# Performance work log

Hardware: AMD Instinct MI355X
Metric: run time of the kernel (lower is better)

The kernel has to match this reference:

```python
import jax, jax.numpy as jnp
from jax import lax
import numpy as np

B, T, I, H, O = 2048, 512, 3, 128, 2


def _uniform(key, shape, scale):
    return jax.random.uniform(key, shape, jnp.float32, -scale, scale)


def setup_inputs() -> dict:
    key = jax.random.key(0)
    ks = jax.random.split(key, 12)
    s = 1.0 / np.sqrt(H)  # PyTorch LSTM init scale
    inp = {
        "x": jax.random.normal(ks[0], (B, T, I), jnp.float32),
        # layer 0: input size I
        "w_ih0": _uniform(ks[1], (4 * H, I), s),
        "w_hh0": _uniform(ks[2], (4 * H, H), s),
        "b_ih0": _uniform(ks[3], (4 * H,), s),
        "b_hh0": _uniform(ks[4], (4 * H,), s),
        # layer 1: input size H
        "w_ih1": _uniform(ks[5], (4 * H, H), s),
        "w_hh1": _uniform(ks[6], (4 * H, H), s),
        "b_ih1": _uniform(ks[7], (4 * H,), s),
        "b_hh1": _uniform(ks[8], (4 * H,), s),
        # final projection
        "fc_w": _uniform(ks[9], (O, H), 1.0 / np.sqrt(H)),
        "fc_b": _uniform(ks[10], (O,), 1.0 / np.sqrt(H)),
    }
    return inp


def _lstm_layer(x, w_ih, w_hh, b_ih, b_hh):
    # x: [B, T, D_in] -> hidden sequence [B, T, H]
    b, t, _ = x.shape
    h_dim = w_hh.shape[1]
    # precompute input projections for all timesteps (one big GEMM)
    x_proj = jnp.einsum("btd,gd->btg", x, w_ih) + b_ih + b_hh  # [B, T, 4H]
    x_proj = jnp.swapaxes(x_proj, 0, 1)  # [T, B, 4H]

    def step(carry, xt):
        h, c = carry
        gates = xt + h @ w_hh.T  # [B, 4H]
        i, f, g, o = jnp.split(gates, 4, axis=-1)  # PyTorch gate order i,f,g,o
        i = jax.nn.sigmoid(i)
        f = jax.nn.sigmoid(f)
        g = jnp.tanh(g)
        o = jax.nn.sigmoid(o)
        c = f * c + i * g
        h = o * jnp.tanh(c)
        return (h, c), h

    h0 = jnp.zeros((b, h_dim), x.dtype)
    c0 = jnp.zeros((b, h_dim), x.dtype)
    _, hs = lax.scan(step, (h0, c0), x_proj)  # hs: [T, B, H]
    return jnp.swapaxes(hs, 0, 1)  # [B, T, H]


def reference(x, w_ih0, w_hh0, b_ih0, b_hh0, w_ih1, w_hh1, b_ih1, b_hh1, fc_w, fc_b):
    h1 = _lstm_layer(x, w_ih0, w_hh0, b_ih0, b_hh0)   # [B, T, H]
    h2 = _lstm_layer(h1, w_ih1, w_hh1, b_ih1, b_hh1)  # [B, T, H]
    last = h2[:, -1, :]                                # [B, H]
    return last @ fc_w.T + fc_b                        # [B, O]
```

## Files before the change

### kernel.cpp

```cpp
#include <hip/hip_runtime.h>

#define B_   2048
#define T_   512
#define H_   128
#define G_   512
#define R_   8
#define NTHR 512

typedef _Float16 f16;
typedef _Float16 f16x8 __attribute__((ext_vector_type(8)));
typedef float    f32x4 __attribute__((ext_vector_type(4)));
typedef int      i32x2 __attribute__((ext_vector_type(2)));

#define OFF_W1    0
#define OFF_RING  131072
#define OFF_HB    139264
#define OFF_XT    143360
#define LDS_BYTES 145408

__device__ __forceinline__ float rcp_(float v) {
#if __has_builtin(__builtin_amdgcn_rcpf)
  return __builtin_amdgcn_rcpf(v);
#else
  return 1.0f / v;
#endif
}
__device__ __forceinline__ float sig_(float v)  { return rcp_(1.0f + __expf(-v)); }
__device__ __forceinline__ float tanh_(float v) { return 1.0f - 2.0f * rcp_(__expf(2.0f * v) + 1.0f); }

__device__ __forceinline__ f16x8 cvt8(const float* __restrict__ p) {
  float4 a = ((const float4*)p)[0];
  float4 b = ((const float4*)p)[1];
  f16x8 v;
  v[0]=(f16)a.x; v[1]=(f16)a.y; v[2]=(f16)a.z; v[3]=(f16)a.w;
  v[4]=(f16)b.x; v[5]=(f16)b.y; v[6]=(f16)b.z; v[7]=(f16)b.w;
  return v;
}
__device__ __forceinline__ f32x4 mfma16(f16x8 a, f16x8 b, f32x4 c) {
  return __builtin_amdgcn_mfma_f32_16x16x32_f16(a, b, c, 0, 0, 0);
}

__device__ __forceinline__ void pls2_(float a, float b, float& x, float& y) {
#if __has_builtin(__builtin_amdgcn_permlane32_swap)
  i32x2 r = __builtin_amdgcn_permlane32_swap(__float_as_int(a), __float_as_int(b),
                                             false, false);
  x = __int_as_float(r.x); y = __int_as_float(r.y);
#else
  asm volatile("v_permlane32_swap_b32 %0, %1" : "+v"(a), "+v"(b));
  x = a; y = b;
#endif
}

__global__ __launch_bounds__(NTHR, 2)
void lstm_v9(const float* __restrict__ x,
             const float* __restrict__ w_ih0, const float* __restrict__ w_hh0,
             const float* __restrict__ b_ih0, const float* __restrict__ b_hh0,
             const float* __restrict__ w_ih1, const float* __restrict__ w_hh1,
             const float* __restrict__ b_ih1, const float* __restrict__ b_hh1,
             const float* __restrict__ fc_w,  const float* __restrict__ fc_b,
             float* __restrict__ out)
{
  extern __shared__ char lds[];
  char*  w1L   = lds + OFF_W1;
  char*  ringB = lds + OFF_RING;
  char*  hBB   = lds + OFF_HB;
  char*  xT    = lds + OFF_XT;

  const int tid  = (int)threadIdx.x;
  const int lane = tid & 63;
  const int wv   = tid >> 6;
  const int n    = lane & 15;
  const int hi   = lane >> 4;
  const int u0   = wv * 16;
  const int blk  = (int)blockIdx.x;
  const int rsw  = (n & 7) << 4;

  for (int idx = tid; idx < G_*16; idx += NTHR) {
    const int g = idx >> 4, s7 = idx & 15;
    f16x8 v = cvt8(w_ih1 + g*H_ + s7*8);
    *(f16x8*)(w1L + g*256 + ((s7*16) ^ ((g&7)<<4))) = v;
  }
  for (int i = tid; i < 3584; i += NTHR) ((unsigned*)ringB)[i] = 0u;
  __syncthreads();

  float xr0 = 0.f, xr1 = 0.f, xr2 = 0.f;
  if (wv == 7) {
    const int tok = lane >> 3, r = lane & 7;
    const size_t base = (size_t)(blk*R_ + r) * T_;
    const float a0 = x[(base + tok)*3+0];
    const float a1 = x[(base + tok)*3+1];
    const float a2 = x[(base + tok)*3+2];
    f16* w = (f16*)(xT + tok*128 + r*16);
    w[0] = (f16)a0; w[1] = (f16)a1; w[2] = (f16)a2;
    xr0 = x[(base + 8 + tok)*3+0];
    xr1 = x[(base + 8 + tok)*3+1];
    xr2 = x[(base + 8 + tok)*3+2];
  }

  f16x8 whh0f[4][4], whh1f[4][4];
  #pragma unroll
  for (int q = 0; q < 4; ++q)
    #pragma unroll
    for (int kc = 0; kc < 4; ++kc) {
      const int off = (q*H_ + u0 + n)*H_ + kc*32 + hi*8;
      whh0f[q][kc] = cvt8(w_hh0 + off);
      whh1f[q][kc] = cvt8(w_hh1 + off);
    }
  f16x8 w0p[4];
  float b0[4], bP[4];
  #pragma unroll
  for (int q = 0; q < 4; ++q) {
    const int g = q*H_ + u0 + n;
    b0[q] = b_ih0[g] + b_hh0[g];
    bP[q] = b_ih1[g] + b_hh1[g];
    f16x8 z;
    #pragma unroll
    for (int e = 0; e < 8; ++e) z[e] = (f16)0.f;
    if (hi == 0) {
      z[0] = (f16)w_ih0[g*3+0];
      z[1] = (f16)w_ih0[g*3+1];
      z[2] = (f16)w_ih0[g*3+2];
    }
    w0p[q] = z;
  }

  int offA[4];
  #pragma unroll
  for (int kc = 0; kc < 4; ++kc)
    offA[kc] = (n&7)*256 + ((kc*64 + hi*16) ^ rsw);
  int offB[4];
  #pragma unroll
  for (int kc = 0; kc < 4; ++kc)
    offB[kc] = (kc*64 + hi*16) ^ rsw;

  float cA0 = 0.f, cA1 = 0.f, cB0 = 0.f, cB1 = 0.f;
  f32x4 xpP[4];
  const int rowbase = (hi & 1)*4 + ((lane >= 32) ? 2 : 0);
  const int colb    = 2*(u0 + n);
  const int wOff0 = rowbase*256     + (colb ^ (rowbase<<4));
  const int wOff1 = (rowbase+1)*256 + (colb ^ ((rowbase+1)<<4));
  __syncthreads();

  auto xstage = [&](int s) {
    if (wv == 7 && (s & 7) == 3) {
      const int c = s >> 3;
      const int tok = lane >> 3, r = lane & 7;
      if (c <= 61) {
        const size_t base = (size_t)(blk*R_ + r) * T_ + (8*(c+2) + tok);
        const float a0 = x[base*3+0], a1 = x[base*3+1], a2 = x[base*3+2];
        f16* w = (f16*)(xT + ((c+1)&1)*1024 + tok*128 + r*16);
        w[0] = (f16)xr0; w[1] = (f16)xr1; w[2] = (f16)xr2;
        xr0 = a0; xr1 = a1; xr2 = a2;
      } else if (c == 62) {
        f16* w = (f16*)(xT + ((c+1)&1)*1024 + tok*128 + r*16);
        w[0] = (f16)xr0; w[1] = (f16)xr1; w[2] = (f16)xr2;
      }
    }
  };

  auto proj = [&](int s) {
    if ((s & 1) == 0 && s >= 2 && s <= T_) {
      const char* pa = ringB + ((n < 8) ? (((s-2)&3)*2048) : (((s-1)&3)*2048));
      #pragma unroll
      for (int q = 0; q < 4; ++q)
        { xpP[q][0]=bP[q]; xpP[q][1]=bP[q]; xpP[q][2]=bP[q]; xpP[q][3]=bP[q]; }
      #pragma unroll
      for (int kc = 0; kc < 4; ++kc) {
        const f16x8 a = *(const f16x8*)(pa + offA[kc]);
        #pragma unroll
        for (int q = 0; q < 4; ++q) {
          const f16x8 bf = *(const f16x8*)(w1L + (q*H_ + u0 + n)*256 + offB[kc]);
          xpP[q] = mfma16(a, bf, xpP[q]);
        }
      }
    }
  };

  auto l0 = [&](int s) {
    if (s < T_) {
      const f16x8 ax = *(const f16x8*)(xT + ((s>>3)&1)*1024 + (s&7)*128 + (n&7)*16);
      f32x4 acc[4];
      #pragma unroll
      for (int q = 0; q < 4; ++q) {
        f32x4 a; a[0]=b0[q]; a[1]=b0[q]; a[2]=b0[q]; a[3]=b0[q];
        acc[q] = mfma16(ax, w0p[q], a);
      }
      const char* pa = ringB + (((s-1)&3)*2048);
      #pragma unroll
      for (int kc = 0; kc < 4; ++kc) {
        const f16x8 af = *(const f16x8*)(pa + offA[kc]);
        #pragma unroll
        for (int q = 0; q < 4; ++q) acc[q] = mfma16(af, whh0f[q][kc], acc[q]);
      }
      char* wr = ringB + ((s&3)*2048);
      float gA[4], gB[4], d0, d1;
      #pragma unroll
      for (int q = 0; q < 4; ++q) {
        pls2_(acc[q][0], acc[q][2], gA[q], d0);
        pls2_(acc[q][1], acc[q][3], gB[q], d1);
      }
      {
        const float iv = sig_(gA[0]), fv = sig_(gA[1]), gv = tanh_(gA[2]), ov = sig_(gA[3]);
        cA0 = fv*cA0 + iv*gv;
        *(f16*)(wr + wOff0) = (f16)(ov * tanh_(cA0));
      }
      {
        const float iv = sig_(gB[0]), fv = sig_(gB[1]), gv = tanh_(gB[2]), ov = sig_(gB[3]);
        cA1 = fv*cA1 + iv*gv;
        *(f16*)(wr + wOff1) = (f16)(ov * tanh_(cA1));
      }
    }
  };

  auto l1 = [&](int s) {
    if (s >= 2) {
      const bool odd = (s & 1);
      const char* pb = hBB + (s&1)*2048;
      f32x4 acc[4];
      #pragma unroll
      for (int q = 0; q < 4; ++q) acc[q] = xpP[q];
      #pragma unroll
      for (int kc = 0; kc < 4; ++kc) {
        const f16x8 af = *(const f16x8*)(pb + offA[kc]);
        #pragma unroll
        for (int q = 0; q < 4; ++q) acc[q] = mfma16(af, whh1f[q][kc], acc[q]);
      }
      char* wr = hBB + (((s+1)&1)*2048);
      float gA[4], gB[4];
      #pragma unroll
      for (int q = 0; q < 4; ++q) {
        float ex, ey, fx, fy;
        pls2_(acc[q][0], acc[q][2], ex, ey);
        pls2_(acc[q][1], acc[q][3], fx, fy);
        gA[q] = odd ? ey : ex;
        gB[q] = odd ? fy : fx;
      }
      {
        const float iv = sig_(gA[0]), fv = sig_(gA[1]), gv = tanh_(gA[2]), ov = sig_(gA[3]);
        cB0 = fv*cB0 + iv*gv;
        *(f16*)(wr + wOff0) = (f16)(ov * tanh_(cB0));
      }
      {
        const float iv = sig_(gB[0]), fv = sig_(gB[1]), gv = tanh_(gB[2]), ov = sig_(gB[3]);
        cB1 = fv*cB1 + iv*gv;
        *(f16*)(wr + wOff1) = (f16)(ov * tanh_(cB1));
      }
    }
  };

  for (int s = 0; s < T_ + 2; ++s) {
    if (wv & 1) {
      xstage(s);
      l0(s);
      proj(s);
      l1(s);
    } else {
      proj(s);
      l1(s);
      l0(s);
    }
    __syncthreads();
  }

  if (tid < R_*2) {
    const int r = tid >> 1, o = tid & 1;
    float acc = fc_b[o];
    #pragma unroll 4
    for (int d = 0; d < H_; ++d) {
      const f16 hv = *(const f16*)(hBB + r*256 + ((2*d) ^ ((r&7)<<4)));
      acc += (float)hv * fc_w[o*H_ + d];
    }
    out[(blk*R_ + r)*2 + o] = acc;
  }
}

extern "C" void kernel_launch(void* const* d_in, const int* in_sizes, int n_in,
                              void* d_out, int out_size, void* d_ws, size_t ws_size,
                              hipStream_t stream) {
  const float* x     = (const float*)d_in[0];
  const float* w_ih0 = (const float*)d_in[1];
  const float* w_hh0 = (const float*)d_in[2];
  const float* b_ih0 = (const float*)d_in[3];
  const float* b_hh0 = (const float*)d_in[4];
  const float* w_ih1 = (const float*)d_in[5];
  const float* w_hh1 = (const float*)d_in[6];
  const float* b_ih1 = (const float*)d_in[7];
  const float* b_hh1 = (const float*)d_in[8];
  const float* fc_w  = (const float*)d_in[9];
  const float* fc_b  = (const float*)d_in[10];
  (void)in_sizes; (void)n_in; (void)out_size; (void)d_ws; (void)ws_size;

  hipFuncSetAttribute((const void*)lstm_v9,
                      hipFuncAttributeMaxDynamicSharedMemorySize, LDS_BYTES);

  lstm_v9<<<B_/R_, NTHR, LDS_BYTES, stream>>>(
      x, w_ih0, w_hh0, b_ih0, b_hh0, w_ih1, w_hh1, b_ih1, b_hh1,
      fc_w, fc_b, (float*)d_out);
}
```

Baseline: 841.5 us.

## Stream fp16 layer-1 input weights from global memory instead of LDS

A small pre-kernel converts w_ih1 to fp16 once into the workspace. The main LSTM kernel then reads those weights from global memory during each layer-1 input projection, rather than copying all 128 KB into a swizzled LDS region at block start. This cuts LDS use from about 145 KB to 14 KB and removes the per-block conversion prologue. The cost is that every projection step now fetches the full weight matrix through the cache hierarchy, which exceeds L1 capacity. Those fetches sit on the recurrent critical path, and the change also adds a second kernel launch.

```diff
diff --git a/kernel.cpp b/kernel.cpp
--- a/kernel.cpp
+++ b/kernel.cpp
@@ -8,15 +8,15 @@
 #define NTHR 512
 
 typedef _Float16 f16;
+typedef _Float16 f16x4 __attribute__((ext_vector_type(4)));
 typedef _Float16 f16x8 __attribute__((ext_vector_type(8)));
 typedef float    f32x4 __attribute__((ext_vector_type(4)));
 typedef int      i32x2 __attribute__((ext_vector_type(2)));
 
-#define OFF_W1    0
-#define OFF_RING  131072
-#define OFF_HB    139264
-#define OFF_XT    143360
-#define LDS_BYTES 145408
+#define OFF_RING  0
+#define OFF_HB    8192
+#define OFF_XT    12288
+#define LDS_BYTES 14336
 
 __device__ __forceinline__ float rcp_(float v) {
 #if __has_builtin(__builtin_amdgcn_rcpf)
@@ -51,17 +51,24 @@
 #endif
 }
 
+__global__ __launch_bounds__(256)
+void cvt_w1(const float* __restrict__ src, f16* __restrict__ dst) {
+  const int i = (int)blockIdx.x * 256 + (int)threadIdx.x;
+  const float4 v = ((const float4*)src)[i];
+  f16x4 o; o[0]=(f16)v.x; o[1]=(f16)v.y; o[2]=(f16)v.z; o[3]=(f16)v.w;
+  ((f16x4*)dst)[i] = o;
+}
+
 __global__ __launch_bounds__(NTHR, 2)
-void lstm_v9(const float* __restrict__ x,
-             const float* __restrict__ w_ih0, const float* __restrict__ w_hh0,
-             const float* __restrict__ b_ih0, const float* __restrict__ b_hh0,
-             const float* __restrict__ w_ih1, const float* __restrict__ w_hh1,
-             const float* __restrict__ b_ih1, const float* __restrict__ b_hh1,
-             const float* __restrict__ fc_w,  const float* __restrict__ fc_b,
-             float* __restrict__ out)
+void lstm_v10(const float* __restrict__ x,
+              const float* __restrict__ w_ih0, const float* __restrict__ w_hh0,
+              const float* __restrict__ b_ih0, const float* __restrict__ b_hh0,
+              const f16*   __restrict__ w1g,   const float* __restrict__ w_hh1,
+              const float* __restrict__ b_ih1, const float* __restrict__ b_hh1,
+              const float* __restrict__ fc_w,  const float* __restrict__ fc_b,
+              float* __restrict__ out)
 {
   extern __shared__ char lds[];
-  char*  w1L   = lds + OFF_W1;
   char*  ringB = lds + OFF_RING;
   char*  hBB   = lds + OFF_HB;
   char*  xT    = lds + OFF_XT;
@@ -75,12 +82,7 @@
   const int blk  = (int)blockIdx.x;
   const int rsw  = (n & 7) << 4;
 
-  for (int idx = tid; idx < G_*16; idx += NTHR) {
-    const int g = idx >> 4, s7 = idx & 15;
-    f16x8 v = cvt8(w_ih1 + g*H_ + s7*8);
-    *(f16x8*)(w1L + g*256 + ((s7*16) ^ ((g&7)<<4))) = v;
-  }
-  for (int i = tid; i < 3584; i += NTHR) ((unsigned*)ringB)[i] = 0u;
+  for (int i = tid; i < 3584; i += NTHR) ((unsigned*)lds)[i] = 0u;
   __syncthreads();
 
   float xr0 = 0.f, xr1 = 0.f, xr2 = 0.f;
@@ -128,10 +130,6 @@
   #pragma unroll
   for (int kc = 0; kc < 4; ++kc)
     offA[kc] = (n&7)*256 + ((kc*64 + hi*16) ^ rsw);
-  int offB[4];
-  #pragma unroll
-  for (int kc = 0; kc < 4; ++kc)
-    offB[kc] = (kc*64 + hi*16) ^ rsw;
 
   float cA0 = 0.f, cA1 = 0.f, cB0 = 0.f, cB1 = 0.f;
   f32x4 xpP[4];
@@ -139,6 +137,7 @@
   const int colb    = 2*(u0 + n);
   const int wOff0 = rowbase*256     + (colb ^ (rowbase<<4));
   const int wOff1 = (rowbase+1)*256 + (colb ^ ((rowbase+1)<<4));
+  const f16* __restrict__ w1base = w1g + (size_t)(u0 + n)*H_ + hi*8;
   __syncthreads();
 
   auto xstage = [&](int s) {
@@ -165,12 +164,22 @@
       for (int q = 0; q < 4; ++q)
         { xpP[q][0]=bP[q]; xpP[q][1]=bP[q]; xpP[q][2]=bP[q]; xpP[q][3]=bP[q]; }
       #pragma unroll
-      for (int kc = 0; kc < 4; ++kc) {
-        const f16x8 a = *(const f16x8*)(pa + offA[kc]);
+      for (int kp = 0; kp < 2; ++kp) {
+        f16x8 bf[2][4];
         #pragma unroll
-        for (int q = 0; q < 4; ++q) {
-          const f16x8 bf = *(const f16x8*)(w1L + (q*H_ + u0 + n)*256 + offB[kc]);
-          xpP[q] = mfma16(a, bf, xpP[q]);
+        for (int kk = 0; kk < 2; ++kk) {
+          const int kc = kp*2 + kk;
+          #pragma unroll
+          for (int q = 0; q < 4; ++q)
+            bf[kk][q] = *(const f16x8*)(w1base + (size_t)q*H_*H_ + kc*32);
+        }
+        #pragma unroll
+        for (int kk = 0; kk < 2; ++kk) {
+          const int kc = kp*2 + kk;
+          const f16x8 a = *(const f16x8*)(pa + offA[kc]);
+          #pragma unroll
+          for (int q = 0; q < 4; ++q)
+            xpP[q] = mfma16(a, bf[kk][q], xpP[q]);
         }
       }
     }
@@ -288,12 +297,13 @@
   const float* b_hh1 = (const float*)d_in[8];
   const float* fc_w  = (const float*)d_in[9];
   const float* fc_b  = (const float*)d_in[10];
-  (void)in_sizes; (void)n_in; (void)out_size; (void)d_ws; (void)ws_size;
-
-  hipFuncSetAttribute((const void*)lstm_v9,
-                      hipFuncAttributeMaxDynamicSharedMemorySize, LDS_BYTES);
-
-  lstm_v9<<<B_/R_, NTHR, LDS_BYTES, stream>>>(
-      x, w_ih0, w_hh0, b_ih0, b_hh0, w_ih1, w_hh1, b_ih1, b_hh1,
+  (void)in_sizes; (void)n_in; (void)out_size; (void)ws_size;
+
+  f16* w1g = (f16*)d_ws;
+
+  cvt_w1<<<G_*H_/4/256, 256, 0, stream>>>(w_ih1, w1g);
+
+  lstm_v10<<<B_/R_, NTHR, LDS_BYTES, stream>>>(
+      x, w_ih0, w_hh0, b_ih0, b_hh0, w1g, w_hh1, b_ih1, b_hh1,
       fc_w, fc_b, (float*)d_out);
 }
```

New measurement: 1.683 ms. +100.0%, slower.
